# Optimization experiments

Hardware: AMD Instinct MI355X
Metric: run time of the kernel (lower is better)

## Reference

```python
import jax, jax.numpy as jnp
import numpy as np

B, P, L = 16, 196, 80
DIM1, DIM2, ATT = 2048, 300, 512
TAU = 1.0


def setup_inputs() -> dict:
    key = jax.random.key(0)
    ks = jax.random.split(key, 8)
    s1 = 1.0 / np.sqrt(DIM1)
    s2 = 1.0 / np.sqrt(DIM2)
    sa = 1.0 / np.sqrt(ATT)
    return {
        "x1": jax.random.normal(ks[0], (B, P, DIM1), dtype=jnp.float32),
        "x2": jax.random.normal(ks[1], (B, L, DIM2), dtype=jnp.float32),
        # nn.Linear weights stored as (out, in), like torch
        "W1": jax.random.uniform(ks[2], (ATT, DIM1), jnp.float32, -s1, s1),
        "W2": jax.random.uniform(ks[3], (ATT, DIM2), jnp.float32, -s2, s2),
        "Wh": jax.random.uniform(ks[4], (ATT, ATT), jnp.float32, -sa, sa),
        "bh": jax.random.uniform(ks[5], (ATT,), jnp.float32, -sa, sa),
        "Wt": jax.random.uniform(ks[6], (1, ATT), jnp.float32, -sa, sa),
        "bt": jax.random.uniform(ks[7], (1,), jnp.float32, -sa, sa),
    }


def reference(x1, x2, W1, W2, Wh, bh, Wt, bt):
    # projections: (B,P,ATT) and (B,L,ATT)
    p1 = jnp.einsum("bpd,ad->bpa", x1, W1)
    p2 = jnp.einsum("bld,ad->bla", x2, W2)
    # broadcast bilinear interaction: (B,L,P,ATT)
    m = jnp.tanh(p1[:, None, :, :] * p2[:, :, None, :])
    h = jnp.einsum("blpa,ca->blpc", m, Wh) + bh
    # score: (B,L,P)
    t = jnp.einsum("blpa,a->blp", h, Wt[0]) + bt[0]
    alpha = jax.nn.softmax(t / TAU, axis=-1)
    # weighted sum over pixels: (B,L,DIM1)
    label_repr = jnp.einsum("blp,bpd->bld", alpha, x1)
    return (label_repr, alpha)
```

## Files before the change

### kernel.cpp

```cpp
#include <hip/hip_runtime.h>

#define B_   16
#define P_   196
#define L_   80
#define DIM1 2048
#define DIM2 300
#define ATT  512

typedef __attribute__((ext_vector_type(8))) short short8x;
typedef __attribute__((ext_vector_type(4))) float f32x4;
typedef __attribute__((ext_vector_type(4))) unsigned int uint4x;
typedef __attribute__((ext_vector_type(4))) unsigned short ushort4x;

__global__ __launch_bounds__(256)
void weff_kernel(const float* __restrict__ Wh, const float* __restrict__ Wt,
                 float* __restrict__ w_eff) {
    __shared__ float part[4][64];
    const int tid = threadIdx.x, lane = tid & 63, quad = tid >> 6;
    const int a = blockIdx.x * 64 + lane;
    float s = 0.f;
    const int c0 = quad * 128;
    for (int c = c0; c < c0 + 128; ++c)
        s = fmaf(Wt[c], Wh[(size_t)c * ATT + a], s);
    part[quad][lane] = s;
    __syncthreads();
    if (tid < 64)
        w_eff[blockIdx.x * 64 + tid] =
            (part[0][tid] + part[1][tid]) + (part[2][tid] + part[3][tid]);
}

__global__ __launch_bounds__(256)
void cvt_bf16_kernel(const float* __restrict__ in, unsigned short* __restrict__ out, int n4) {
    for (int i = blockIdx.x * 256 + threadIdx.x; i < n4; i += gridDim.x * 256) {
        uint4x u = ((const uint4x*)in)[i];
        ushort4x o;
        #pragma unroll
        for (int j = 0; j < 4; ++j) {
            unsigned v = u[j];
            v += 0x7fffu + ((v >> 16) & 1u);
            o[j] = (unsigned short)(v >> 16);
        }
        ((ushort4x*)out)[i] = o;
    }
}

#define GM 3136
#define GN 512
#define GK 2048

__device__ __forceinline__ void gload16(const unsigned short* g, unsigned short* l) {
    __builtin_amdgcn_global_load_lds(
        (const __attribute__((address_space(1))) unsigned int*)g,
        (__attribute__((address_space(3))) unsigned int*)l, 16, 0, 0);
}

__global__ __launch_bounds__(256)
void gemm_bf16_mfma(const unsigned short* __restrict__ Ab,
                    const unsigned short* __restrict__ Bb,
                    float* __restrict__ C) {
    __shared__ unsigned short As[2][64 * 64];
    __shared__ unsigned short Bs[2][64 * 64];
    const int tid  = threadIdx.x;
    const int wid  = tid >> 6;
    const int lane = tid & 63;
    const int bm   = blockIdx.x * 64;
    const int bn   = blockIdx.y * 64;
    const int wm   = wid >> 1;
    const int wn   = wid & 1;

    const int srow = lane >> 3;
    const int scol = ((lane & 7) ^ srow) << 3;
    const size_t arow0 = (size_t)(bm + (wid << 4) + srow) * GK;
    const size_t brow0 = (size_t)(bn + (wid << 4) + srow) * GK;

#define STAGE_TILE(buf, k0)                                                        \
    {                                                                              \
        gload16(Ab + arow0 + (k0) + scol,            &As[buf][((wid << 4) + 0) * 64]); \
        gload16(Ab + arow0 + (size_t)8 * GK + (k0) + scol, &As[buf][((wid << 4) + 8) * 64]); \
        gload16(Bb + brow0 + (k0) + scol,            &Bs[buf][((wid << 4) + 0) * 64]); \
        gload16(Bb + brow0 + (size_t)8 * GK + (k0) + scol, &Bs[buf][((wid << 4) + 8) * 64]); \
    }

    f32x4 acc[2][2] = {};
    const int fr  = lane & 15;
    const int kb  = (lane >> 4) << 3;
    const int swz = (lane & 7) << 4;

    STAGE_TILE(0, 0)
    constexpr int NT = GK / 64;
    for (int kt = 0; kt < NT; ++kt) {
        __syncthreads();
        if (kt + 1 < NT) STAGE_TILE((kt + 1) & 1, (kt + 1) * 64)
        const char* pa = (const char*)&As[kt & 1][0];
        const char* pb = (const char*)&Bs[kt & 1][0];
        #pragma unroll
        for (int kk = 0; kk < 2; ++kk) {
            const int koff = ((kk * 32 + kb) * 2) ^ swz;
            short8x a[2], b[2];
            #pragma unroll
            for (int m = 0; m < 2; ++m)
                a[m] = *(const short8x*)(pa + (wm * 32 + m * 16 + fr) * 128 + koff);
            #pragma unroll
            for (int n = 0; n < 2; ++n)
                b[n] = *(const short8x*)(pb + (wn * 32 + n * 16 + fr) * 128 + koff);
            #pragma unroll
            for (int m = 0; m < 2; ++m)
                #pragma unroll
                for (int n = 0; n < 2; ++n)
                    acc[m][n] = __builtin_amdgcn_mfma_f32_16x16x32_bf16(a[m], b[n], acc[m][n], 0, 0, 0);
        }
        __syncthreads();
    }

    const int crow = (lane >> 4) << 2;
    #pragma unroll
    for (int m = 0; m < 2; ++m)
        #pragma unroll
        for (int n = 0; n < 2; ++n)
            #pragma unroll
            for (int j = 0; j < 4; ++j)
                C[(size_t)(bm + wm * 32 + m * 16 + crow + j) * GN + bn + wn * 32 + n * 16 + fr] =
                    acc[m][n][j];
#undef STAGE_TILE
}

__global__ __launch_bounds__(256)
void gemm_nt(const float* __restrict__ A, const float* __restrict__ Bm,
             float* __restrict__ C, int M, int N, int K) {
    constexpr int BK = 16;
    __shared__ float As[BK][64];
    __shared__ float Bs[BK][64];
    const int tid  = threadIdx.x;
    const int bm   = blockIdx.x * 64;
    const int bn   = blockIdx.y * 64;
    const int ty   = tid >> 4;
    const int tx   = tid & 15;
    const int lrow = tid >> 2;
    const int lc4  = (tid & 3) << 2;
    float acc[4][4] = {};
    const float* Arow = A  + (size_t)(bm + lrow) * K;
    const float* Brow = Bm + (size_t)(bn + lrow) * K;

    for (int k0 = 0; k0 < K; k0 += BK) {
        float4 av, bv;
        if (k0 + BK <= K) {
            av = *(const float4*)(Arow + k0 + lc4);
            bv = *(const float4*)(Brow + k0 + lc4);
        } else {
            float a_[4], b_[4];
            #pragma unroll
            for (int i = 0; i < 4; ++i) {
                const int k = k0 + lc4 + i;
                a_[i] = (k < K) ? Arow[k] : 0.f;
                b_[i] = (k < K) ? Brow[k] : 0.f;
            }
            av = make_float4(a_[0], a_[1], a_[2], a_[3]);
            bv = make_float4(b_[0], b_[1], b_[2], b_[3]);
        }
        __syncthreads();
        As[lc4 + 0][lrow] = av.x;
        As[lc4 + 1][lrow] = av.y;
        As[lc4 + 2][lrow] = av.z;
        As[lc4 + 3][lrow] = av.w;
        Bs[lc4 + 0][lrow] = bv.x;
        Bs[lc4 + 1][lrow] = bv.y;
        Bs[lc4 + 2][lrow] = bv.z;
        Bs[lc4 + 3][lrow] = bv.w;
        __syncthreads();
        #pragma unroll
        for (int k = 0; k < BK; ++k) {
            const float4 a4 = *(const float4*)&As[k][ty << 2];
            const float4 b4 = *(const float4*)&Bs[k][tx << 2];
            const float ae[4] = {a4.x, a4.y, a4.z, a4.w};
            const float be[4] = {b4.x, b4.y, b4.z, b4.w};
            #pragma unroll
            for (int i = 0; i < 4; ++i)
                #pragma unroll
                for (int j = 0; j < 4; ++j)
                    acc[i][j] = fmaf(ae[i], be[j], acc[i][j]);
        }
    }
    #pragma unroll
    for (int i = 0; i < 4; ++i) {
        float4 o = make_float4(acc[i][0], acc[i][1], acc[i][2], acc[i][3]);
        *(float4*)(C + (size_t)(bm + (ty << 2) + i) * N + bn + (tx << 2)) = o;
    }
}

#define LOG2E2 2.8853900817779268f

__global__ __launch_bounds__(256)
void score_softmax_kernel(const float* __restrict__ p1, const float* __restrict__ p2,
                          const float* __restrict__ w_eff, float* __restrict__ alpha) {
    const int bidx = blockIdx.x;
    const int bl = (bidx & 7) * 160 + (bidx >> 3);
    const int b  = bl / L_;
    __shared__ float s_t[P_];
    __shared__ float s_red[4];
    const int tid = threadIdx.x, wave = tid >> 6, lane = tid & 63;

    const float4* gp2 = (const float4*)(p2 + (size_t)bl * ATT);
    const float4* gw  = (const float4*)w_eff;
    const float4 q0 = gp2[lane], q1 = gp2[64 + lane];
    const float4 w0 = gw[lane],  w1 = gw[64 + lane];
    float qa[8] = {q0.x * LOG2E2, q0.y * LOG2E2, q0.z * LOG2E2, q0.w * LOG2E2,
                   q1.x * LOG2E2, q1.y * LOG2E2, q1.z * LOG2E2, q1.w * LOG2E2};
    float wa[8] = {w0.x, w0.y, w0.z, w0.w, w1.x, w1.y, w1.z, w1.w};

    const float* p1b = p1 + (size_t)b * P_ * ATT;
    for (int p = wave; p < P_; p += 4) {
        const float4* row = (const float4*)(p1b + (size_t)p * ATT);
        const float4 r0 = row[lane], r1 = row[64 + lane];
        const float rr[8] = {r0.x, r0.y, r0.z, r0.w, r1.x, r1.y, r1.z, r1.w};
        float acc = 0.f;
        #pragma unroll
        for (int j = 0; j < 8; ++j) {
            const float e = __builtin_amdgcn_exp2f(rr[j] * qa[j]);
            acc = fmaf(wa[j], __builtin_amdgcn_rcpf(e + 1.f), acc);
        }
        #pragma unroll
        for (int off = 32; off >= 1; off >>= 1) acc += __shfl_xor(acc, off);
        if (lane == 0) s_t[p] = acc;
    }
    __syncthreads();
    const float v = (tid < P_) ? -2.f * s_t[tid] : -1e30f;
    float m = v;
    #pragma unroll
    for (int off = 32; off >= 1; off >>= 1) m = fmaxf(m, __shfl_xor(m, off));
    if (lane == 0) s_red[wave] = m;
    __syncthreads();
    m = fmaxf(fmaxf(s_red[0], s_red[1]), fmaxf(s_red[2], s_red[3]));
    __syncthreads();
    const float e = (tid < P_) ? __expf(v - m) : 0.f;
    float s = e;
    #pragma unroll
    for (int off = 32; off >= 1; off >>= 1) s += __shfl_xor(s, off);
    if (lane == 0) s_red[wave] = s;
    __syncthreads();
    s = s_red[0] + s_red[1] + s_red[2] + s_red[3];
    if (tid < P_) alpha[(size_t)bl * P_ + tid] = e / s;
}

__global__ __launch_bounds__(256)
void label_kernel(const float* __restrict__ alpha, const float* __restrict__ x1,
                  float* __restrict__ out) {
    const int dt = blockIdx.x;
    const int lt = blockIdx.y;
    const int b  = blockIdx.z;
    __shared__ float s_alpha[P_][16];
    const int tid = threadIdx.x;
    for (int idx = tid; idx < 16 * P_; idx += 256) {
        const int p = idx >> 4, i = idx & 15;
        s_alpha[p][i] = alpha[(size_t)(b * L_ + lt * 16 + i) * P_ + p];
    }
    __syncthreads();
    const int d = dt * 256 + tid;
    const float* xcol = x1 + (size_t)b * P_ * DIM1 + d;
    float acc[16] = {};
    for (int p = 0; p < P_; p += 4) {
        float xv[4];
        #pragma unroll
        for (int u = 0; u < 4; ++u) xv[u] = xcol[(size_t)(p + u) * DIM1];
        #pragma unroll
        for (int u = 0; u < 4; ++u) {
            const float4 a0 = *(const float4*)&s_alpha[p + u][0];
            const float4 a1 = *(const float4*)&s_alpha[p + u][4];
            const float4 a2 = *(const float4*)&s_alpha[p + u][8];
            const float4 a3 = *(const float4*)&s_alpha[p + u][12];
            acc[0]  = fmaf(a0.x, xv[u], acc[0]);
            acc[1]  = fmaf(a0.y, xv[u], acc[1]);
            acc[2]  = fmaf(a0.z, xv[u], acc[2]);
            acc[3]  = fmaf(a0.w, xv[u], acc[3]);
            acc[4]  = fmaf(a1.x, xv[u], acc[4]);
            acc[5]  = fmaf(a1.y, xv[u], acc[5]);
            acc[6]  = fmaf(a1.z, xv[u], acc[6]);
            acc[7]  = fmaf(a1.w, xv[u], acc[7]);
            acc[8]  = fmaf(a2.x, xv[u], acc[8]);
            acc[9]  = fmaf(a2.y, xv[u], acc[9]);
            acc[10] = fmaf(a2.z, xv[u], acc[10]);
            acc[11] = fmaf(a2.w, xv[u], acc[11]);
            acc[12] = fmaf(a3.x, xv[u], acc[12]);
            acc[13] = fmaf(a3.y, xv[u], acc[13]);
            acc[14] = fmaf(a3.z, xv[u], acc[14]);
            acc[15] = fmaf(a3.w, xv[u], acc[15]);
        }
    }
    #pragma unroll
    for (int i = 0; i < 16; ++i)
        out[(size_t)(b * L_ + lt * 16 + i) * DIM1 + d] = acc[i];
}

extern "C" void kernel_launch(void* const* d_in, const int* in_sizes, int n_in,
                              void* d_out, int out_size, void* d_ws, size_t ws_size,
                              hipStream_t stream) {
    const float* x1 = (const float*)d_in[0];
    const float* x2 = (const float*)d_in[1];
    const float* W1 = (const float*)d_in[2];
    const float* W2 = (const float*)d_in[3];
    const float* Wh = (const float*)d_in[4];
    const float* Wt = (const float*)d_in[6];

    float* ws    = (float*)d_ws;
    float* p1    = ws;
    float* p2    = p1 + (size_t)B_ * P_ * ATT;
    float* w_eff = p2 + (size_t)B_ * L_ * ATT;
    unsigned short* x1b = (unsigned short*)(w_eff + ATT);
    unsigned short* W1b = x1b + (size_t)B_ * P_ * DIM1;

    float* label = (float*)d_out;
    float* alpha = label + (size_t)B_ * L_ * DIM1;

    hipLaunchKernelGGL(cvt_bf16_kernel, dim3(2048), dim3(256), 0, stream,
                       x1, x1b, (B_ * P_ * DIM1) / 4);
    hipLaunchKernelGGL(cvt_bf16_kernel, dim3(512), dim3(256), 0, stream,
                       W1, W1b, (ATT * DIM1) / 4);
    hipLaunchKernelGGL(weff_kernel, dim3(8), dim3(256), 0, stream, Wh, Wt, w_eff);
    hipLaunchKernelGGL(gemm_nt, dim3((B_ * L_) / 64, ATT / 64), dim3(256), 0, stream,
                       x2, W2, p2, B_ * L_, ATT, DIM2);
    hipLaunchKernelGGL(gemm_bf16_mfma, dim3(GM / 64, GN / 64), dim3(256), 0, stream,
                       x1b, W1b, p1);
    hipLaunchKernelGGL(score_softmax_kernel, dim3(B_ * L_), dim3(256), 0, stream,
                       p1, p2, w_eff, alpha);
    hipLaunchKernelGGL(label_kernel, dim3(8, 5, B_), dim3(256), 0, stream,
                       alpha, x1, label);
}
```

Before: 204.1 us.

## Pair tanh terms to halve reciprocals, prefetch rows, narrow bf16 GEMM tiles

```diff
diff --git a/kernel.cpp b/kernel.cpp
--- a/kernel.cpp
+++ b/kernel.cpp
@@ -59,29 +59,26 @@
                     const unsigned short* __restrict__ Bb,
                     float* __restrict__ C) {
     __shared__ unsigned short As[2][64 * 64];
-    __shared__ unsigned short Bs[2][64 * 64];
+    __shared__ unsigned short Bs[2][32 * 64];
     const int tid  = threadIdx.x;
     const int wid  = tid >> 6;
     const int lane = tid & 63;
     const int bm   = blockIdx.x * 64;
-    const int bn   = blockIdx.y * 64;
-    const int wm   = wid >> 1;
-    const int wn   = wid & 1;
+    const int bn   = blockIdx.y * 32;
 
     const int srow = lane >> 3;
     const int scol = ((lane & 7) ^ srow) << 3;
     const size_t arow0 = (size_t)(bm + (wid << 4) + srow) * GK;
-    const size_t brow0 = (size_t)(bn + (wid << 4) + srow) * GK;
-
-#define STAGE_TILE(buf, k0)                                                        \
-    {                                                                              \
-        gload16(Ab + arow0 + (k0) + scol,            &As[buf][((wid << 4) + 0) * 64]); \
+    const size_t brow0 = (size_t)(bn + (wid << 3) + srow) * GK;
+
+#define STAGE_TILE(buf, k0)                                                              \
+    {                                                                                    \
+        gload16(Ab + arow0 + (k0) + scol,                  &As[buf][((wid << 4) + 0) * 64]); \
         gload16(Ab + arow0 + (size_t)8 * GK + (k0) + scol, &As[buf][((wid << 4) + 8) * 64]); \
-        gload16(Bb + brow0 + (k0) + scol,            &Bs[buf][((wid << 4) + 0) * 64]); \
-        gload16(Bb + brow0 + (size_t)8 * GK + (k0) + scol, &Bs[buf][((wid << 4) + 8) * 64]); \
-    }
-
-    f32x4 acc[2][2] = {};
+        gload16(Bb + brow0 + (k0) + scol,                  &Bs[buf][(wid << 3) * 64]);       \
+    }
+
+    f32x4 acc[2] = {};
     const int fr  = lane & 15;
     const int kb  = (lane >> 4) << 3;
     const int swz = (lane & 7) << 4;
@@ -96,31 +93,24 @@
         #pragma unroll
         for (int kk = 0; kk < 2; ++kk) {
             const int koff = ((kk * 32 + kb) * 2) ^ swz;
-            short8x a[2], b[2];
-            #pragma unroll
-            for (int m = 0; m < 2; ++m)
-                a[m] = *(const short8x*)(pa + (wm * 32 + m * 16 + fr) * 128 + koff);
+            short8x a = *(const short8x*)(pa + ((wid << 4) + fr) * 128 + koff);
+            short8x b[2];
             #pragma unroll
             for (int n = 0; n < 2; ++n)
-                b[n] = *(const short8x*)(pb + (wn * 32 + n * 16 + fr) * 128 + koff);
-            #pragma unroll
-            for (int m = 0; m < 2; ++m)
-                #pragma unroll
-                for (int n = 0; n < 2; ++n)
-                    acc[m][n] = __builtin_amdgcn_mfma_f32_16x16x32_bf16(a[m], b[n], acc[m][n], 0, 0, 0);
+                b[n] = *(const short8x*)(pb + (n * 16 + fr) * 128 + koff);
+            #pragma unroll
+            for (int n = 0; n < 2; ++n)
+                acc[n] = __builtin_amdgcn_mfma_f32_16x16x32_bf16(a, b[n], acc[n], 0, 0, 0);
         }
         __syncthreads();
     }
 
     const int crow = (lane >> 4) << 2;
     #pragma unroll
-    for (int m = 0; m < 2; ++m)
-        #pragma unroll
-        for (int n = 0; n < 2; ++n)
-            #pragma unroll
-            for (int j = 0; j < 4; ++j)
-                C[(size_t)(bm + wm * 32 + m * 16 + crow + j) * GN + bn + wn * 32 + n * 16 + fr] =
-                    acc[m][n][j];
+    for (int n = 0; n < 2; ++n)
+        #pragma unroll
+        for (int j = 0; j < 4; ++j)
+            C[(size_t)(bm + (wid << 4) + crow + j) * GN + bn + n * 16 + fr] = acc[n][j];
 #undef STAGE_TILE
 }
 
@@ -198,29 +188,58 @@
     __shared__ float s_t[P_];
     __shared__ float s_red[4];
     const int tid = threadIdx.x, wave = tid >> 6, lane = tid & 63;
+    const int g = lane >> 4, c = lane & 15;
 
     const float4* gp2 = (const float4*)(p2 + (size_t)bl * ATT);
     const float4* gw  = (const float4*)w_eff;
-    const float4 q0 = gp2[lane], q1 = gp2[64 + lane];
-    const float4 w0 = gw[lane],  w1 = gw[64 + lane];
-    float qa[8] = {q0.x * LOG2E2, q0.y * LOG2E2, q0.z * LOG2E2, q0.w * LOG2E2,
-                   q1.x * LOG2E2, q1.y * LOG2E2, q1.z * LOG2E2, q1.w * LOG2E2};
-    float wa[8] = {w0.x, w0.y, w0.z, w0.w, w1.x, w1.y, w1.z, w1.w};
+    float4 qa[8], wa[8];
+    #pragma unroll
+    for (int j = 0; j < 8; ++j) {
+        const float4 q = gp2[c + 16 * j];
+        qa[j] = make_float4(q.x * LOG2E2, q.y * LOG2E2, q.z * LOG2E2, q.w * LOG2E2);
+        wa[j] = gw[c + 16 * j];
+    }
 
     const float* p1b = p1 + (size_t)b * P_ * ATT;
-    for (int p = wave; p < P_; p += 4) {
-        const float4* row = (const float4*)(p1b + (size_t)p * ATT);
-        const float4 r0 = row[lane], r1 = row[64 + lane];
-        const float rr[8] = {r0.x, r0.y, r0.z, r0.w, r1.x, r1.y, r1.z, r1.w};
+    const int nch = (wave == 0) ? 13 : 12;
+    int p = 16 * 0 + 4 * wave + g;
+    int ptail = 192 + g;
+    int row0 = (0 < 12) ? p : ptail;
+    float4 cur[8], nxt[8];
+    {
+        const float4* row = (const float4*)(p1b + (size_t)row0 * ATT);
+        #pragma unroll
+        for (int j = 0; j < 8; ++j) cur[j] = row[c + 16 * j];
+    }
+    for (int i = 0; i < nch; ++i) {
+        const int pr = (i < 12) ? (16 * i + 4 * wave + g) : ptail;
+        if (i + 1 < nch) {
+            const int pn = (i + 1 < 12) ? (16 * (i + 1) + 4 * wave + g) : ptail;
+            const float4* row = (const float4*)(p1b + (size_t)pn * ATT);
+            #pragma unroll
+            for (int j = 0; j < 8; ++j) nxt[j] = row[c + 16 * j];
+        }
         float acc = 0.f;
         #pragma unroll
         for (int j = 0; j < 8; ++j) {
-            const float e = __builtin_amdgcn_exp2f(rr[j] * qa[j]);
-            acc = fmaf(wa[j], __builtin_amdgcn_rcpf(e + 1.f), acc);
-        }
-        #pragma unroll
-        for (int off = 32; off >= 1; off >>= 1) acc += __shfl_xor(acc, off);
-        if (lane == 0) s_t[p] = acc;
+            const float e0 = __builtin_amdgcn_exp2f(cur[j].x * qa[j].x);
+            const float e1 = __builtin_amdgcn_exp2f(cur[j].y * qa[j].y);
+            const float e2 = __builtin_amdgcn_exp2f(cur[j].z * qa[j].z);
+            const float e3 = __builtin_amdgcn_exp2f(cur[j].w * qa[j].w);
+            float num = fmaf(wa[j].x, e1, fmaf(wa[j].y, e0, wa[j].x + wa[j].y));
+            float den = fmaf(e0, e1, e0 + e1 + 1.f);
+            acc = fmaf(num, __builtin_amdgcn_rcpf(den), acc);
+            num = fmaf(wa[j].z, e3, fmaf(wa[j].w, e2, wa[j].z + wa[j].w));
+            den = fmaf(e2, e3, e2 + e3 + 1.f);
+            acc = fmaf(num, __builtin_amdgcn_rcpf(den), acc);
+        }
+        acc += __shfl_xor(acc, 1);
+        acc += __shfl_xor(acc, 2);
+        acc += __shfl_xor(acc, 4);
+        acc += __shfl_xor(acc, 8);
+        if (c == 0) s_t[pr] = acc;
+        #pragma unroll
+        for (int j = 0; j < 8; ++j) cur[j] = nxt[j];
     }
     __syncthreads();
     const float v = (tid < P_) ? -2.f * s_t[tid] : -1e30f;
@@ -317,7 +336,7 @@
     hipLaunchKernelGGL(weff_kernel, dim3(8), dim3(256), 0, stream, Wh, Wt, w_eff);
     hipLaunchKernelGGL(gemm_nt, dim3((B_ * L_) / 64, ATT / 64), dim3(256), 0, stream,
                        x2, W2, p2, B_ * L_, ATT, DIM2);
-    hipLaunchKernelGGL(gemm_bf16_mfma, dim3(GM / 64, GN / 64), dim3(256), 0, stream,
+    hipLaunchKernelGGL(gemm_bf16_mfma, dim3(GM / 64, GN / 32), dim3(256), 0, stream,
                        x1b, W1b, p1);
     hipLaunchKernelGGL(score_softmax_kernel, dim3(B_ * L_), dim3(256), 0, stream,
                        p1, p2, w_eff, alpha);
```

Result: faster. 196.9 us (-3.5%).
